# Optimization experiments

Hardware: AMD Instinct MI355X
Metric: run time of the kernel (lower is better)

Reference implementation:

```python
import jax, jax.numpy as jnp
import numpy as np

N, E = 20000, 320000          # nodes, edges (avg in-degree ~16)
F_IN, EMB, T, OUT = 40, 40, 5, 2
F_T = EMB // T                # per-tower output width = 8
EPS_STD, EPS_GN = 1e-5, 1e-5


def _lin_init(k, fan_in, fan_out, extra=()):
    return jax.random.normal(k, (*extra, fan_in, fan_out), jnp.float32) / np.sqrt(fan_in)


def setup_inputs() -> dict:
    key = jax.random.key(0)
    ks = jax.random.split(key, 8)
    # deg histogram in init: all 20000 nodes with degree 16 -> avg_deg['log'] = log(16+1)
    return dict(
        x=jax.random.normal(ks[0], (N, F_IN), jnp.float32),
        edge_index=jax.random.randint(ks[1], (2, E), 0, N),
        W_pre=_lin_init(ks[2], 2 * F_IN, F_IN, (T,)),   # per-tower pre-MLP
        b_pre=jnp.zeros((T, F_IN), jnp.float32),
        W_post=_lin_init(ks[3], 13 * F_IN, F_T, (T,)),  # (4 agg * 3 scalers + 1 residual) * F_in
        b_post=jnp.zeros((T, F_T), jnp.float32),
        W_lin=_lin_init(ks[4], T * F_T, EMB),           # PNAConv final mixing linear
        b_lin=jnp.zeros((EMB,), jnp.float32),
        gn_weight=jnp.ones((EMB,), jnp.float32),
        gn_bias=jnp.zeros((EMB,), jnp.float32),
        gn_mean_scale=jnp.ones((EMB,), jnp.float32),
        W1=_lin_init(ks[5], EMB, EMB),                  # head hidden linear
        b1=jnp.zeros((EMB,), jnp.float32),
        W2=_lin_init(ks[6], EMB, OUT),                  # head output linear
        b2=jnp.zeros((OUT,), jnp.float32),
        avg_deg_log=jnp.float32(np.log(17.0)),
    )


def _pna_conv(x, src, dst, W_pre, b_pre, W_post, b_post, W_lin, b_lin, avg_deg_log):
    xi, xj = x[dst], x[src]                              # gather: [E, F]
    h = jnp.concatenate([xi, xj], axis=-1)               # [E, 2F]
    m = jnp.einsum('ef,tfg->etg', h, W_pre) + b_pre      # per-tower messages [E, T, F]
    cnt = jax.ops.segment_sum(jnp.ones((E,), m.dtype), dst, num_segments=N)  # in-degree [N]
    denom = jnp.maximum(cnt, 1.0)[:, None, None]
    mean = jax.ops.segment_sum(m, dst, num_segments=N) / denom
    mean2 = jax.ops.segment_sum(m * m, dst, num_segments=N) / denom
    std = jnp.sqrt(jax.nn.relu(mean2 - mean * mean) + EPS_STD)
    has = (cnt > 0)[:, None, None]
    mn = jnp.where(has, jax.ops.segment_min(m, dst, num_segments=N), 0.0)
    mx = jnp.where(has, jax.ops.segment_max(m, dst, num_segments=N), 0.0)
    agg = jnp.concatenate([mean, mn, mx, std], axis=-1)  # [N, T, 4F]
    deg = jnp.maximum(cnt, 1.0)[:, None, None]
    logd = jnp.log(deg + 1.0)
    out = jnp.concatenate(
        [agg, agg * (logd / avg_deg_log), agg * (avg_deg_log / logd)], axis=-1)  # [N, T, 12F]
    out = jnp.concatenate(
        [jnp.broadcast_to(x[:, None, :], (N, T, x.shape[-1])), out], axis=-1)    # [N, T, 13F]
    out = jnp.einsum('ntf,tfg->ntg', out, W_post) + b_post                       # [N, T, F_T]
    return out.reshape(N, T * F_T) @ W_lin + b_lin


def _graph_norm(x, w, b, mean_scale):
    mean = jnp.mean(x, axis=0, keepdims=True)
    out = x - mean_scale * mean
    var = jnp.mean(out * out, axis=0, keepdims=True)
    return w * out / jnp.sqrt(var + EPS_GN) + b


def reference(x, edge_index, W_pre, b_pre, W_post, b_post, W_lin, b_lin,
              gn_weight, gn_bias, gn_mean_scale, W1, b1, W2, b2, avg_deg_log):
    src, dst = edge_index[0], edge_index[1]
    h = _pna_conv(x, src, dst, W_pre, b_pre, W_post, b_post, W_lin, b_lin, avg_deg_log)
    h = jax.nn.relu(_graph_norm(h, gn_weight, gn_bias, gn_mean_scale))
    h = jax.nn.relu(h @ W1 + b1)   # dropout_rate=None -> no dropout
    return h @ W2 + b2
```

## Files before the change

kernel.cpp:

```cpp
#include <hip/hip_runtime.h>
#include <math.h>

#define N_NODES 20000
#define N_EDGES 320000
#define F_IN 40
#define T_TOW 5
#define EMB 40
#define NPB_PRE 16
#define NBLK_MIX 313
#define PLANE (T_TOW * N_NODES * 40)
#define ECHUNK 16
#define STRIDE 64

typedef __attribute__((ext_vector_type(8))) _Float16 half8;
typedef __attribute__((ext_vector_type(2))) _Float16 half2_t;

#define WS_STATS   0
#define WS_CURSOR  320
#define WS_SSRC    80384
#define WS_MS      5200384
#define WS_MD      13200384
#define WS_AGG     21200384
#define WS_XPOST   53200384
#define WS_H0T     69200384
#define WS_PART    72400384

__global__ __launch_bounds__(256) void k_pre(const float* __restrict__ x,
                                             const float* __restrict__ W_pre,
                                             const float* __restrict__ b_pre,
                                             const float* __restrict__ W_post,
                                             const float* __restrict__ b_post,
                                             _Float16* __restrict__ mS,
                                             _Float16* __restrict__ mD,
                                             float* __restrict__ xpostT,
                                             int* __restrict__ cursor) {
  const int tid = threadIdx.x;
  const int n0 = blockIdx.x * NPB_PRE;
  if (tid < NPB_PRE) cursor[n0 + tid] = (n0 + tid) * STRIDE;
  const bool statlane = tid < 200;
  const int q = tid - 200;
  const bool xplane = (q >= 0 && q < 40);
  const int tc = statlane ? tid : 199;
  const int t = tc / 40, g = tc - t * 40;
  const int t2 = xplane ? q / 8 : 0, g2 = xplane ? q - (q / 8) * 8 : 0;
  float wA[40], wB[40];
  const float* Wt = W_pre + t * 3200;
#pragma unroll
  for (int j = 0; j < 40; ++j) {
    wA[j] = statlane ? Wt[j * 40 + g] : W_post[t2 * 4160 + j * 8 + g2];
    wB[j] = statlane ? Wt[(40 + j) * 40 + g] : 0.f;
  }
  const float bias = statlane ? b_pre[t * 40 + g] : b_post[t2 * 8 + g2];
  for (int ni = 0; ni < NPB_PRE; ++ni) {
    const int n = n0 + ni;
    const float* xr = x + n * F_IN;
    float aA = bias, aB = 0.f;
#pragma unroll
    for (int j = 0; j < 40; j += 4) {
      const float4 xv = *(const float4*)(xr + j);
      aA += xv.x * wA[j] + xv.y * wA[j + 1] + xv.z * wA[j + 2] + xv.w * wA[j + 3];
      aB += xv.x * wB[j] + xv.y * wB[j + 1] + xv.z * wB[j + 2] + xv.w * wB[j + 3];
    }
    if (statlane) {
      mD[n * 200 + tc] = (_Float16)aA;
      mS[n * 200 + tc] = (_Float16)aB;
    } else if (xplane) {
      xpostT[t2 * (N_NODES * 8) + n * 8 + g2] = aA;
    }
  }
}

__global__ __launch_bounds__(256) void k_scatter(const int* __restrict__ src,
                                                 const int* __restrict__ dst,
                                                 int* __restrict__ cursor,
                                                 int* __restrict__ ssrc) {
  int i = blockIdx.x * 256 + threadIdx.x;
  if (i < N_EDGES) {
    int d = dst[i];
    int pos = atomicAdd(&cursor[d], 1);
    ssrc[pos] = src[i];
  }
}

__global__ __launch_bounds__(256) void k_edge(const _Float16* __restrict__ mS,
                                              const _Float16* __restrict__ mD,
                                              const int* __restrict__ cursor,
                                              const int* __restrict__ ssrc,
                                              _Float16* __restrict__ aggS) {
  const int lane = threadIdx.x & 63;
  const int wv = threadIdx.x >> 6;
  const int n = blockIdx.x * 4 + wv;
  const int r0 = n * STRIDE;
  const int r1 = __builtin_amdgcn_readfirstlane(cursor[n]);
  const int cnt = r1 - r0;
  const int cpa = lane;
  const bool bact = lane < 36;
  const int cpb = bact ? 64 + lane : 99;
  const half2_t mda = ((const half2_t*)(mD + n * 200))[cpa];
  const half2_t mdb = ((const half2_t*)(mD + n * 200))[cpb];

  const _Float16 HINF = (_Float16)65504.f;
  half2_t suma = {0, 0}, ssqa = {0, 0}, sumb = {0, 0}, ssqb = {0, 0};
  half2_t mna = {HINF, HINF}, mxa = {-HINF, -HINF};
  half2_t mnb = {HINF, HINF}, mxb = {-HINF, -HINF};
  half2_t va = {0, 0}, vb = {0, 0};

  if (cnt > 0) {
    for (int p = r0; p < r1; p += ECHUNK) {
      half2_t ha[ECHUNK], hb[ECHUNK];
#pragma unroll
      for (int i = 0; i < ECHUNK; ++i) {
        const int qe = (p + i < r1) ? (p + i) : (r1 - 1);
        const int s = __builtin_amdgcn_readfirstlane(ssrc[qe]);
        const half2_t* row = (const half2_t*)(mS + s * 200);
        ha[i] = row[cpa];
        hb[i] = row[cpb];
      }
#pragma unroll
      for (int i = 0; i < ECHUNK; ++i) {
        suma += ha[i];
        ssqa += ha[i] * ha[i];
        mna = __builtin_elementwise_min(mna, ha[i]);
        mxa = __builtin_elementwise_max(mxa, ha[i]);
        sumb += hb[i];
        ssqb += hb[i] * hb[i];
        mnb = __builtin_elementwise_min(mnb, hb[i]);
        mxb = __builtin_elementwise_max(mxb, hb[i]);
      }
      va = ha[ECHUNK - 1];
      vb = hb[ECHUNK - 1];
    }
  }

  const int padded = ((cnt + ECHUNK - 1) / ECHUNK) * ECHUNK;
  const float d = (float)(padded - cnt);
  const float inv = (cnt > 0) ? 1.f / (float)cnt : 0.f;
#pragma unroll
  for (int set = 0; set < 2; ++set) {
    if (set == 1 && !bact) break;
    const int cp = set == 0 ? cpa : cpb;
    const half2_t sum2 = set == 0 ? suma : sumb;
    const half2_t ssq2 = set == 0 ? ssqa : ssqb;
    const half2_t mn2 = set == 0 ? mna : mnb;
    const half2_t mx2 = set == 0 ? mxa : mxb;
    const half2_t vl2 = set == 0 ? va : vb;
    const half2_t md2 = set == 0 ? mda : mdb;
    half2_t omean, omn, omx, osd;
#pragma unroll
    for (int j = 0; j < 2; ++j) {
      float mean, mnf, mxf, sd;
      if (cnt > 0) {
        const float vl = (float)vl2[j];
        const float sf = (float)sum2[j] - d * vl;
        const float qf = (float)ssq2[j] - d * vl * vl;
        const float msm = sf * inv;
        const float var = qf * inv - msm * msm;
        sd = sqrtf(fmaxf(var, 0.f) + 1e-5f);
        const float mdf = (float)md2[j];
        mean = mdf + msm;
        mnf = mdf + (float)mn2[j];
        mxf = mdf + (float)mx2[j];
      } else {
        mean = 0.f; mnf = 0.f; mxf = 0.f; sd = sqrtf(1e-5f);
      }
      omean[j] = (_Float16)mean;
      omn[j] = (_Float16)mnf;
      omx[j] = (_Float16)mxf;
      osd[j] = (_Float16)sd;
    }
    const int t = cp / 20, g = 2 * (cp - t * 20);
    half2_t* a = (half2_t*)(aggS + (t * N_NODES + n) * 40 + g);
    a[0] = omean;
    *(half2_t*)((_Float16*)a + PLANE) = omn;
    *(half2_t*)((_Float16*)a + 2 * PLANE) = omx;
    *(half2_t*)((_Float16*)a + 3 * PLANE) = osd;
  }
}

__global__ __launch_bounds__(256) void k_postmix(const _Float16* __restrict__ aggS,
                                                 const int* __restrict__ cursor,
                                                 const float* __restrict__ W_post,
                                                 const float* __restrict__ avg_dl,
                                                 const float* __restrict__ xpostT,
                                                 const float* __restrict__ W_lin,
                                                 const float* __restrict__ b_lin,
                                                 float* __restrict__ h0T,
                                                 float* __restrict__ partial) {
  __shared__ float sPost[4][64 * 41];
  __shared__ float sP[64 * 41];
  const int tid = threadIdx.x;
  const int wv = tid >> 6, lane = tid & 63;
  const int n0 = blockIdx.x * 64;
  const int n = n0 + lane;
  const bool ok = n < N_NODES;
  const int nn = ok ? n : N_NODES - 1;
  const int st = __builtin_amdgcn_readfirstlane(wv);
  const int cnt = cursor[nn] - nn * STRIDE;
  const float degf = fmaxf((float)cnt, 1.f);
  const float logd = logf(degf + 1.f);
  const float avg = avg_dl[0];
  const float s1v = logd / avg, s2v = avg / logd;

  half8 cur[5], nx[5];
  {
    const half8* ar = (const half8*)(aggS + st * PLANE + nn * 40);
#pragma unroll
    for (int q2 = 0; q2 < 5; ++q2) cur[q2] = ar[q2];
  }
  for (int t = 0; t < 5; ++t) {
    if (t < 4) {
      const half8* ar = (const half8*)(aggS + st * PLANE + ((t + 1) * N_NODES + nn) * 40);
#pragma unroll
      for (int q2 = 0; q2 < 5; ++q2) nx[q2] = ar[q2];
    }
    const float* Wt = W_post + t * 4160 + (40 + st * 40) * 8;
    float A[8], B[8], C[8];
#pragma unroll
    for (int g = 0; g < 8; ++g) { A[g] = 0.f; B[g] = 0.f; C[g] = 0.f; }
#pragma unroll
    for (int f = 0; f < 40; ++f) {
      const float val = (float)cur[f >> 3][f & 7];
      const float* wrow = Wt + f * 8;
#pragma unroll
      for (int g = 0; g < 8; ++g) {
        A[g] = fmaf(val, wrow[g], A[g]);
        B[g] = fmaf(val, wrow[1280 + g], B[g]);
        C[g] = fmaf(val, wrow[2560 + g], C[g]);
      }
    }
    float* dstp = &sPost[st][lane * 41 + t * 8];
#pragma unroll
    for (int g = 0; g < 8; ++g) dstp[g] = A[g] + s1v * B[g] + s2v * C[g];
    if (t < 4) {
#pragma unroll
      for (int q2 = 0; q2 < 5; ++q2) cur[q2] = nx[q2];
    }
  }
  __syncthreads();

#pragma unroll
  for (int i = 0; i < 10; ++i) {
    const int c = wv + 4 * i;
    const int t2 = c >> 3, g2 = c & 7;
    float v = 0.f;
    if (ok) {
      v = xpostT[t2 * (N_NODES * 8) + n * 8 + g2]
        + sPost[0][lane * 41 + c] + sPost[1][lane * 41 + c]
        + sPost[2][lane * 41 + c] + sPost[3][lane * 41 + c];
    }
    sP[lane * 41 + c] = v;
  }
  __syncthreads();

  for (int c = wv; c < 5; c += 4) {
    const int c0 = c * 8;
    const float4 bb0 = *(const float4*)(b_lin + c0);
    const float4 bb1 = *(const float4*)(b_lin + c0 + 4);
    float a0 = bb0.x, a1 = bb0.y, a2 = bb0.z, a3 = bb0.w;
    float a4 = bb1.x, a5 = bb1.y, a6 = bb1.z, a7 = bb1.w;
    for (int k = 0; k < 40; ++k) {
      const float p = sP[lane * 41 + k];
      const float* w = W_lin + k * EMB + c0;
      const float4 w0 = *(const float4*)(w);
      const float4 w1 = *(const float4*)(w + 4);
      a0 = fmaf(p, w0.x, a0); a1 = fmaf(p, w0.y, a1);
      a2 = fmaf(p, w0.z, a2); a3 = fmaf(p, w0.w, a3);
      a4 = fmaf(p, w1.x, a4); a5 = fmaf(p, w1.y, a5);
      a6 = fmaf(p, w1.z, a6); a7 = fmaf(p, w1.w, a7);
    }
    if (ok) {
      h0T[(c0 + 0) * N_NODES + n] = a0;
      h0T[(c0 + 1) * N_NODES + n] = a1;
      h0T[(c0 + 2) * N_NODES + n] = a2;
      h0T[(c0 + 3) * N_NODES + n] = a3;
      h0T[(c0 + 4) * N_NODES + n] = a4;
      h0T[(c0 + 5) * N_NODES + n] = a5;
      h0T[(c0 + 6) * N_NODES + n] = a6;
      h0T[(c0 + 7) * N_NODES + n] = a7;
    } else {
      a0 = a1 = a2 = a3 = a4 = a5 = a6 = a7 = 0.f;
    }
    float red[8] = {a0, a1, a2, a3, a4, a5, a6, a7};
#pragma unroll
    for (int j = 0; j < 8; ++j) {
      float sv = red[j], qv = red[j] * red[j];
#pragma unroll
      for (int m = 32; m >= 1; m >>= 1) {
        sv += __shfl_xor(sv, m, 64);
        qv += __shfl_xor(qv, m, 64);
      }
      if (lane == 0) {
        partial[blockIdx.x * 80 + c0 + j] = sv;
        partial[blockIdx.x * 80 + 40 + c0 + j] = qv;
      }
    }
  }
}

__global__ __launch_bounds__(256) void k_head(const float* __restrict__ partial,
                                              const float* __restrict__ h0T,
                                              const float* __restrict__ gn_w,
                                              const float* __restrict__ gn_b,
                                              const float* __restrict__ gn_ms,
                                              const float* __restrict__ W1,
                                              const float* __restrict__ b1,
                                              const float* __restrict__ W2,
                                              const float* __restrict__ b2,
                                              float* __restrict__ out) {
  __shared__ float sV[64 * 41];
  __shared__ float sH[64 * 41];
  __shared__ float sS[3][80];
  const int tid = threadIdx.x;
  const int n0 = blockIdx.x * 64;
  const float invN = 1.f / (float)N_NODES;
  if (tid < 240) {
    const int chunk = tid / 80;
    const int col = tid - chunk * 80;
    const int b0 = chunk * 105;
    const int b1 = (chunk == 2) ? NBLK_MIX : b0 + 105;
    float a0 = 0.f, a1 = 0.f, a2 = 0.f, a3 = 0.f;
    int b = b0;
    for (; b + 4 <= b1; b += 4) {
      a0 += partial[(b + 0) * 80 + col];
      a1 += partial[(b + 1) * 80 + col];
      a2 += partial[(b + 2) * 80 + col];
      a3 += partial[(b + 3) * 80 + col];
    }
    for (; b < b1; ++b) a0 += partial[b * 80 + col];
    sS[chunk][col] = (a0 + a1) + (a2 + a3);
  }
  __syncthreads();
  for (int i = 0; i < 10; ++i) {
    const int idx = tid + i * 256;
    const int e = idx >> 6, r = idx & 63;
    const int nn0 = n0 + r;
    const int nn = (nn0 < N_NODES) ? nn0 : 0;
    const float S1e = sS[0][e] + sS[1][e] + sS[2][e];
    const float S2e = sS[0][40 + e] + sS[1][40 + e] + sS[2][40 + e];
    const float M = S1e * invN;
    const float ms = gn_ms[e];
    const float var = S2e * invN - ms * (2.f - ms) * M * M;
    const float sc = gn_w[e] / sqrtf(var + 1e-5f);
    const float he = h0T[e * N_NODES + nn];
    sV[r * 41 + e] = fmaxf((he - ms * M) * sc + gn_b[e], 0.f);
  }
  __syncthreads();
  const int wv = tid >> 6, lane = tid & 63;
  const int c0 = wv * 10;
  float acc[10];
#pragma unroll
  for (int j = 0; j < 10; ++j) acc[j] = b1[c0 + j];
  for (int k = 0; k < 40; ++k) {
    const float p = sV[lane * 41 + k];
    const float* w = W1 + k * EMB + c0;
#pragma unroll
    for (int j = 0; j < 10; ++j) acc[j] = fmaf(p, w[j], acc[j]);
  }
#pragma unroll
  for (int j = 0; j < 10; ++j) sH[lane * 41 + c0 + j] = fmaxf(acc[j], 0.f);
  __syncthreads();
  if (tid < 64) {
    const int n = n0 + tid;
    if (n < N_NODES) {
      float o0 = b2[0], o1 = b2[1];
      const float* hr = sH + tid * 41;
#pragma unroll
      for (int k = 0; k < 40; ++k) {
        const float r = hr[k];
        o0 = fmaf(r, W2[k * 2], o0);
        o1 = fmaf(r, W2[k * 2 + 1], o1);
      }
      out[n * 2] = o0;
      out[n * 2 + 1] = o1;
    }
  }
}

extern "C" void kernel_launch(void* const* d_in, const int* in_sizes, int n_in,
                              void* d_out, int out_size, void* d_ws, size_t ws_size,
                              hipStream_t stream) {
  const float* x      = (const float*)d_in[0];
  const int*   ei     = (const int*)d_in[1];
  const float* W_pre  = (const float*)d_in[2];
  const float* b_pre  = (const float*)d_in[3];
  const float* W_post = (const float*)d_in[4];
  const float* b_post = (const float*)d_in[5];
  const float* W_lin  = (const float*)d_in[6];
  const float* b_lin  = (const float*)d_in[7];
  const float* gn_w   = (const float*)d_in[8];
  const float* gn_b   = (const float*)d_in[9];
  const float* gn_ms  = (const float*)d_in[10];
  const float* W1     = (const float*)d_in[11];
  const float* b1     = (const float*)d_in[12];
  const float* W2     = (const float*)d_in[13];
  const float* b2     = (const float*)d_in[14];
  const float* avg_dl = (const float*)d_in[15];
  float* out = (float*)d_out;

  char* ws = (char*)d_ws;
  int* cursor = (int*)(ws + WS_CURSOR);
  int* ssrc   = (int*)(ws + WS_SSRC);
  _Float16* mS   = (_Float16*)(ws + WS_MS);
  _Float16* mD   = (_Float16*)(ws + WS_MD);
  _Float16* aggS = (_Float16*)(ws + WS_AGG);
  float* xpostT  = (float*)(ws + WS_XPOST);
  float* h0T     = (float*)(ws + WS_H0T);
  float* part    = (float*)(ws + WS_PART);
  const int* e_src = ei;
  const int* e_dst = ei + N_EDGES;

  k_pre<<<N_NODES / NPB_PRE, 256, 0, stream>>>(x, W_pre, b_pre, W_post, b_post,
                                               mS, mD, xpostT, cursor);
  k_scatter<<<(N_EDGES + 255) / 256, 256, 0, stream>>>(e_src, e_dst, cursor, ssrc);
  k_edge<<<N_NODES / 4, 256, 0, stream>>>(mS, mD, cursor, ssrc, aggS);
  k_postmix<<<NBLK_MIX, 256, 0, stream>>>(aggS, cursor, W_post, avg_dl,
                                          xpostT, W_lin, b_lin, h0T, part);
  k_head<<<NBLK_MIX, 256, 0, stream>>>(part, h0T, gn_w, gn_b, gn_ms,
                                       W1, b1, W2, b2, out);
}
```

Before: 218.4 us.

## Repartition postmix across towers and stats, add separate partial-stats reduction kernel

The post-aggregation kernel now handles 16 nodes per block with 320 threads. Each wave owns one tower and lanes are split over the four aggregator statistics, whose results are combined with cross-lane shuffles instead of a shared-memory staging array. This makes 1250 blocks instead of 313, which should fill the GPU better and cut per-thread serial work and LDS use. Because there are now many more partial-sum rows, a new small kernel reduces the GraphNorm partials, and the head kernel reads those totals, at the cost of one extra launch.

```diff
diff --git a/kernel.cpp b/kernel.cpp
--- a/kernel.cpp
+++ b/kernel.cpp
@@ -8,6 +8,8 @@
 #define EMB 40
 #define NPB_PRE 16
 #define NBLK_MIX 313
+#define NPB_PM 16
+#define NBLK_PM 1250
 #define PLANE (T_TOW * N_NODES * 40)
 #define ECHUNK 16
 #define STRIDE 64
@@ -177,7 +179,7 @@
   }
 }
 
-__global__ __launch_bounds__(256) void k_postmix(const _Float16* __restrict__ aggS,
+__global__ __launch_bounds__(320) void k_postmix(const _Float16* __restrict__ aggS,
                                                  const int* __restrict__ cursor,
                                                  const float* __restrict__ W_post,
                                                  const float* __restrict__ avg_dl,
@@ -186,118 +188,107 @@
                                                  const float* __restrict__ b_lin,
                                                  float* __restrict__ h0T,
                                                  float* __restrict__ partial) {
-  __shared__ float sPost[4][64 * 41];
-  __shared__ float sP[64 * 41];
+  __shared__ float sP[16 * 41];
   const int tid = threadIdx.x;
-  const int wv = tid >> 6, lane = tid & 63;
-  const int n0 = blockIdx.x * 64;
-  const int n = n0 + lane;
-  const bool ok = n < N_NODES;
-  const int nn = ok ? n : N_NODES - 1;
-  const int st = __builtin_amdgcn_readfirstlane(wv);
-  const int cnt = cursor[nn] - nn * STRIDE;
+  const int t = tid >> 6;
+  const int l = tid & 63;
+  const int s = l >> 4;
+  const int ni = l & 15;
+  const int n0 = blockIdx.x * NPB_PM;
+  const int n = n0 + ni;
+
+  const int cnt = cursor[n] - n * STRIDE;
   const float degf = fmaxf((float)cnt, 1.f);
   const float logd = logf(degf + 1.f);
   const float avg = avg_dl[0];
   const float s1v = logd / avg, s2v = avg / logd;
 
-  half8 cur[5], nx[5];
+  half8 cur[5];
   {
-    const half8* ar = (const half8*)(aggS + st * PLANE + nn * 40);
+    const half8* ar = (const half8*)(aggS + s * PLANE + ((size_t)t * N_NODES + n) * 40);
 #pragma unroll
     for (int q2 = 0; q2 < 5; ++q2) cur[q2] = ar[q2];
   }
-  for (int t = 0; t < 5; ++t) {
-    if (t < 4) {
-      const half8* ar = (const half8*)(aggS + st * PLANE + ((t + 1) * N_NODES + nn) * 40);
-#pragma unroll
-      for (int q2 = 0; q2 < 5; ++q2) nx[q2] = ar[q2];
-    }
-    const float* Wt = W_post + t * 4160 + (40 + st * 40) * 8;
-    float A[8], B[8], C[8];
-#pragma unroll
-    for (int g = 0; g < 8; ++g) { A[g] = 0.f; B[g] = 0.f; C[g] = 0.f; }
-#pragma unroll
-    for (int f = 0; f < 40; ++f) {
-      const float val = (float)cur[f >> 3][f & 7];
-      const float* wrow = Wt + f * 8;
-#pragma unroll
-      for (int g = 0; g < 8; ++g) {
-        A[g] = fmaf(val, wrow[g], A[g]);
-        B[g] = fmaf(val, wrow[1280 + g], B[g]);
-        C[g] = fmaf(val, wrow[2560 + g], C[g]);
-      }
-    }
-    float* dstp = &sPost[st][lane * 41 + t * 8];
-#pragma unroll
-    for (int g = 0; g < 8; ++g) dstp[g] = A[g] + s1v * B[g] + s2v * C[g];
-    if (t < 4) {
-#pragma unroll
-      for (int q2 = 0; q2 < 5; ++q2) cur[q2] = nx[q2];
-    }
+  const float* Wt = W_post + t * 4160 + (40 + s * 40) * 8;
+  float A[8], B[8], C[8];
+#pragma unroll
+  for (int g = 0; g < 8; ++g) { A[g] = 0.f; B[g] = 0.f; C[g] = 0.f; }
+#pragma unroll
+  for (int f = 0; f < 40; ++f) {
+    const float val = (float)cur[f >> 3][f & 7];
+    const float* wrow = Wt + f * 8;
+#pragma unroll
+    for (int g = 0; g < 8; ++g) {
+      A[g] = fmaf(val, wrow[g], A[g]);
+      B[g] = fmaf(val, wrow[1280 + g], B[g]);
+      C[g] = fmaf(val, wrow[2560 + g], C[g]);
+    }
+  }
+  float v[8];
+#pragma unroll
+  for (int g = 0; g < 8; ++g) {
+    v[g] = A[g] + s1v * B[g] + s2v * C[g];
+    v[g] += __shfl_xor(v[g], 16, 64);
+    v[g] += __shfl_xor(v[g], 32, 64);
+  }
+  if (s == 0) {
+    const float* xp = xpostT + t * (N_NODES * 8) + n * 8;
+#pragma unroll
+    for (int g = 0; g < 8; ++g) sP[ni * 41 + t * 8 + g] = v[g] + xp[g];
   }
   __syncthreads();
 
-#pragma unroll
-  for (int i = 0; i < 10; ++i) {
-    const int c = wv + 4 * i;
-    const int t2 = c >> 3, g2 = c & 7;
-    float v = 0.f;
-    if (ok) {
-      v = xpostT[t2 * (N_NODES * 8) + n * 8 + g2]
-        + sPost[0][lane * 41 + c] + sPost[1][lane * 41 + c]
-        + sPost[2][lane * 41 + c] + sPost[3][lane * 41 + c];
-    }
-    sP[lane * 41 + c] = v;
-  }
+  const int cq = l & 3;
+  const int nb = l >> 2;
+  const int nB = n0 + nb;
+  const int cc = t * 8 + cq * 2;
+  float a0 = b_lin[cc], a1 = b_lin[cc + 1];
+  for (int k = 0; k < 40; ++k) {
+    const float p = sP[nb * 41 + k];
+    const float2 w = *(const float2*)(W_lin + k * EMB + cc);
+    a0 = fmaf(p, w.x, a0);
+    a1 = fmaf(p, w.y, a1);
+  }
+  h0T[cc * N_NODES + nB] = a0;
+  h0T[(cc + 1) * N_NODES + nB] = a1;
+  float q0 = a0 * a0, q1 = a1 * a1;
+#pragma unroll
+  for (int m = 4; m <= 32; m <<= 1) {
+    a0 += __shfl_xor(a0, m, 64);
+    a1 += __shfl_xor(a1, m, 64);
+    q0 += __shfl_xor(q0, m, 64);
+    q1 += __shfl_xor(q1, m, 64);
+  }
+  if (nb == 0) {
+    float* pb = partial + blockIdx.x * 80;
+    pb[cc] = a0;
+    pb[cc + 1] = a1;
+    pb[40 + cc] = q0;
+    pb[40 + cc + 1] = q1;
+  }
+}
+
+__global__ __launch_bounds__(256) void k_stats(const float* __restrict__ partial,
+                                               float* __restrict__ S1,
+                                               float* __restrict__ S2) {
+  const int col = blockIdx.x;
+  const int tid = threadIdx.x;
+  __shared__ float red[4];
+  float s = 0.f;
+  for (int b = tid; b < NBLK_PM; b += 256) s += partial[b * 80 + col];
+#pragma unroll
+  for (int m = 32; m >= 1; m >>= 1) s += __shfl_xor(s, m, 64);
+  if ((tid & 63) == 0) red[tid >> 6] = s;
   __syncthreads();
-
-  for (int c = wv; c < 5; c += 4) {
-    const int c0 = c * 8;
-    const float4 bb0 = *(const float4*)(b_lin + c0);
-    const float4 bb1 = *(const float4*)(b_lin + c0 + 4);
-    float a0 = bb0.x, a1 = bb0.y, a2 = bb0.z, a3 = bb0.w;
-    float a4 = bb1.x, a5 = bb1.y, a6 = bb1.z, a7 = bb1.w;
-    for (int k = 0; k < 40; ++k) {
-      const float p = sP[lane * 41 + k];
-      const float* w = W_lin + k * EMB + c0;
-      const float4 w0 = *(const float4*)(w);
-      const float4 w1 = *(const float4*)(w + 4);
-      a0 = fmaf(p, w0.x, a0); a1 = fmaf(p, w0.y, a1);
-      a2 = fmaf(p, w0.z, a2); a3 = fmaf(p, w0.w, a3);
-      a4 = fmaf(p, w1.x, a4); a5 = fmaf(p, w1.y, a5);
-      a6 = fmaf(p, w1.z, a6); a7 = fmaf(p, w1.w, a7);
-    }
-    if (ok) {
-      h0T[(c0 + 0) * N_NODES + n] = a0;
-      h0T[(c0 + 1) * N_NODES + n] = a1;
-      h0T[(c0 + 2) * N_NODES + n] = a2;
-      h0T[(c0 + 3) * N_NODES + n] = a3;
-      h0T[(c0 + 4) * N_NODES + n] = a4;
-      h0T[(c0 + 5) * N_NODES + n] = a5;
-      h0T[(c0 + 6) * N_NODES + n] = a6;
-      h0T[(c0 + 7) * N_NODES + n] = a7;
-    } else {
-      a0 = a1 = a2 = a3 = a4 = a5 = a6 = a7 = 0.f;
-    }
-    float red[8] = {a0, a1, a2, a3, a4, a5, a6, a7};
-#pragma unroll
-    for (int j = 0; j < 8; ++j) {
-      float sv = red[j], qv = red[j] * red[j];
-#pragma unroll
-      for (int m = 32; m >= 1; m >>= 1) {
-        sv += __shfl_xor(sv, m, 64);
-        qv += __shfl_xor(qv, m, 64);
-      }
-      if (lane == 0) {
-        partial[blockIdx.x * 80 + c0 + j] = sv;
-        partial[blockIdx.x * 80 + 40 + c0 + j] = qv;
-      }
-    }
-  }
-}
-
-__global__ __launch_bounds__(256) void k_head(const float* __restrict__ partial,
+  if (tid == 0) {
+    const float tot = (red[0] + red[1]) + (red[2] + red[3]);
+    if (col < 40) S1[col] = tot;
+    else S2[col - 40] = tot;
+  }
+}
+
+__global__ __launch_bounds__(256) void k_head(const float* __restrict__ S1,
+                                              const float* __restrict__ S2,
                                               const float* __restrict__ h0T,
                                               const float* __restrict__ gn_w,
                                               const float* __restrict__ gn_b,
@@ -309,37 +300,17 @@
                                               float* __restrict__ out) {
   __shared__ float sV[64 * 41];
   __shared__ float sH[64 * 41];
-  __shared__ float sS[3][80];
   const int tid = threadIdx.x;
   const int n0 = blockIdx.x * 64;
   const float invN = 1.f / (float)N_NODES;
-  if (tid < 240) {
-    const int chunk = tid / 80;
-    const int col = tid - chunk * 80;
-    const int b0 = chunk * 105;
-    const int b1 = (chunk == 2) ? NBLK_MIX : b0 + 105;
-    float a0 = 0.f, a1 = 0.f, a2 = 0.f, a3 = 0.f;
-    int b = b0;
-    for (; b + 4 <= b1; b += 4) {
-      a0 += partial[(b + 0) * 80 + col];
-      a1 += partial[(b + 1) * 80 + col];
-      a2 += partial[(b + 2) * 80 + col];
-      a3 += partial[(b + 3) * 80 + col];
-    }
-    for (; b < b1; ++b) a0 += partial[b * 80 + col];
-    sS[chunk][col] = (a0 + a1) + (a2 + a3);
-  }
-  __syncthreads();
   for (int i = 0; i < 10; ++i) {
     const int idx = tid + i * 256;
     const int e = idx >> 6, r = idx & 63;
     const int nn0 = n0 + r;
     const int nn = (nn0 < N_NODES) ? nn0 : 0;
-    const float S1e = sS[0][e] + sS[1][e] + sS[2][e];
-    const float S2e = sS[0][40 + e] + sS[1][40 + e] + sS[2][40 + e];
-    const float M = S1e * invN;
+    const float M = S1[e] * invN;
     const float ms = gn_ms[e];
-    const float var = S2e * invN - ms * (2.f - ms) * M * M;
+    const float var = S2[e] * invN - ms * (2.f - ms) * M * M;
     const float sc = gn_w[e] / sqrtf(var + 1e-5f);
     const float he = h0T[e * N_NODES + nn];
     sV[r * 41 + e] = fmaxf((he - ms * M) * sc + gn_b[e], 0.f);
@@ -398,6 +369,8 @@
   float* out = (float*)d_out;
 
   char* ws = (char*)d_ws;
+  float* S1   = (float*)(ws + WS_STATS);
+  float* S2   = S1 + 40;
   int* cursor = (int*)(ws + WS_CURSOR);
   int* ssrc   = (int*)(ws + WS_SSRC);
   _Float16* mS   = (_Float16*)(ws + WS_MS);
@@ -413,8 +386,9 @@
                                                mS, mD, xpostT, cursor);
   k_scatter<<<(N_EDGES + 255) / 256, 256, 0, stream>>>(e_src, e_dst, cursor, ssrc);
   k_edge<<<N_NODES / 4, 256, 0, stream>>>(mS, mD, cursor, ssrc, aggS);
-  k_postmix<<<NBLK_MIX, 256, 0, stream>>>(aggS, cursor, W_post, avg_dl,
-                                          xpostT, W_lin, b_lin, h0T, part);
-  k_head<<<NBLK_MIX, 256, 0, stream>>>(part, h0T, gn_w, gn_b, gn_ms,
+  k_postmix<<<NBLK_PM, 320, 0, stream>>>(aggS, cursor, W_post, avg_dl,
+                                         xpostT, W_lin, b_lin, h0T, part);
+  k_stats<<<80, 256, 0, stream>>>(part, S1, S2);
+  k_head<<<NBLK_MIX, 256, 0, stream>>>(S1, S2, h0T, gn_w, gn_b, gn_ms,
                                        W1, b1, W2, b2, out);
 }
```

After: 237.5 us. 8.7% more time.
